# Optimization experiments

Hardware: AMD Instinct MI355X
Metric: run time of the kernel (lower is better)

Reference implementation:

```python
import jax, jax.numpy as jnp
import numpy as np
from jax import lax

V, Dm, NL, N, K, E = 32000, 1024, 4, 16, 4, 2
Di = Dm * E
B, T = 1, 2048
EPS = 1e-5


def setup_inputs() -> dict:
    key = jax.random.key(0)
    ks = jax.random.split(key, 8)
    s = 0.02
    A_init = jnp.log(jnp.arange(1.0, N + 1, dtype=jnp.float32))  # (N,)
    return {
        "idx": jax.random.randint(ks[0], (B, T), 0, V),
        "emb": jax.random.normal(ks[1], (V, Dm), dtype=jnp.float32) * s,
        "norm_w": jnp.ones((NL, Dm), jnp.float32),
        "in_proj_w": jax.random.normal(ks[2], (NL, 2 * Di, Dm), dtype=jnp.float32) * s,
        "conv_w": jax.random.normal(ks[3], (NL, Di, 1, K), dtype=jnp.float32) * s,
        "conv_b": jnp.zeros((NL, Di), jnp.float32),
        "x_proj_w": jax.random.normal(ks[4], (NL, 2 * N + 1, Di), dtype=jnp.float32) * s,
        "dt_proj_w": jax.random.normal(ks[5], (NL, Di, 1), dtype=jnp.float32) * s,
        "dt_proj_b": jnp.zeros((NL, Di), jnp.float32),
        "A_log": jnp.broadcast_to(A_init[None, None, :], (NL, Di, N)).copy(),
        "D_param": jnp.ones((NL, Di), jnp.float32),
        "out_proj_w": jax.random.normal(ks[6], (NL, Dm, Di), dtype=jnp.float32) * s,
        "norm_f_w": jnp.ones((Dm,), jnp.float32),
    }


def _rmsnorm(x, w):
    rms = jnp.sqrt(jnp.mean(x * x, axis=-1, keepdims=True) + EPS)
    return x / rms * w


def _mamba_block(x, in_w, cw, cb, xp_w, dt_w, dt_b, A_log, Dp, out_w):
    # x: (B, L, Dm)
    xz = x @ in_w.T                       # (B, L, 2*Di)
    x_ssm, z = xz[..., :Di], xz[..., Di:]
    # causal depthwise conv (torch pads both sides then crops -> left-pad only)
    xc = x_ssm.transpose(0, 2, 1)         # (B, Di, L)
    xc = lax.conv_general_dilated(
        xc, cw, window_strides=(1,), padding=[(K - 1, 0)],
        dimension_numbers=("NCH", "OIH", "NCH"), feature_group_count=Di)
    xc = xc + cb[None, :, None]
    u = jax.nn.silu(xc.transpose(0, 2, 1))  # (B, L, Di)
    # selective SSM
    A = -jnp.exp(A_log)                     # (Di, N)
    xp = u @ xp_w.T                         # (B, L, 2N+1)
    dt_raw, Bv, Cv = xp[..., :1], xp[..., 1:1 + N], xp[..., 1 + N:]
    dt = jax.nn.softplus(dt_raw * dt_w[:, 0] + dt_b)  # (B, L, Di)

    def step(h, inp):
        dt_t, Bv_t, Cv_t, u_t = inp          # (B,Di),(B,N),(B,N),(B,Di)
        dA = jnp.exp(dt_t[..., None] * A)    # (B, Di, N)
        h = dA * h + (dt_t * u_t)[..., None] * Bv_t[:, None, :]
        y_t = jnp.einsum("bdn,bn->bd", h, Cv_t)
        return h, y_t

    h0 = jnp.zeros((x.shape[0], Di, N), u.dtype)
    xs = (dt.transpose(1, 0, 2), Bv.transpose(1, 0, 2),
          Cv.transpose(1, 0, 2), u.transpose(1, 0, 2))
    _, ys = lax.scan(step, h0, xs)           # (L, B, Di)
    y = ys.transpose(1, 0, 2) + u * Dp
    y = y * jax.nn.silu(z)
    return y @ out_w.T


def reference(idx, emb, norm_w, in_proj_w, conv_w, conv_b, x_proj_w,
              dt_proj_w, dt_proj_b, A_log, D_param, out_proj_w, norm_f_w):
    x = emb[idx]                             # (B, T, Dm); dropout=0 in eval
    for l in range(NL):
        x = x + _mamba_block(_rmsnorm(x, norm_w[l]), in_proj_w[l], conv_w[l],
                             conv_b[l], x_proj_w[l], dt_proj_w[l], dt_proj_b[l],
                             A_log[l], D_param[l], out_proj_w[l])
    x = _rmsnorm(x, norm_f_w)
    logits = x @ emb.T                       # tied lm_head
    return logits
```

## Files before the change

kernel.cpp:

```cpp
#include <hip/hip_runtime.h>
#include <hip/hip_bf16.h>

typedef __hip_bfloat16 bf16;
typedef __attribute__((ext_vector_type(8))) short short8;
typedef __attribute__((ext_vector_type(4))) float f32x4;

#define TT 2048
#define DM 1024
#define DI 2048
#define NLAYER 4
#define NST 16
#define KC 4
#define VOCAB 32000
#define XPS 33
#define NCHUNK 64
#define CLEN 32

__device__ __forceinline__ float us2f(unsigned short u) {
    union { float f; unsigned int i; } c; c.i = ((unsigned int)u) << 16; return c.f;
}
__device__ __forceinline__ float ldin(const void* p, size_t i, int f32) {
    return f32 ? ((const float*)p)[i] : us2f(((const unsigned short*)p)[i]);
}
__device__ __forceinline__ unsigned short f2us(float f) {
    bf16 h = __float2bfloat16(f);
    return *(unsigned short*)&h;
}
__device__ __forceinline__ size_t hidx(int n, int c, int d) {
    return ((size_t)n * NCHUNK + c) * DI + d;
}

__global__ void detect_kernel(const unsigned int* __restrict__ w_bits, int* __restrict__ flag) {
    if (threadIdx.x == 0) *flag = (w_bits[0] == 0x3F800000u) ? 1 : 0;
}

__global__ void cvt8_dual_kernel(const float* __restrict__ sA, unsigned short* __restrict__ dA, int n8A,
                                 const float* __restrict__ sB, unsigned short* __restrict__ dB, int n8B) {
    int i = blockIdx.x * 256 + threadIdx.x;
    const float* s; unsigned short* d;
    if (i < n8A) { s = sA; d = dA; }
    else { i -= n8A; if (i >= n8B) return; s = sB; d = dB; }
    float4 a = ((const float4*)s)[2 * i];
    float4 b = ((const float4*)s)[2 * i + 1];
    unsigned int w0 = (unsigned int)f2us(a.x) | ((unsigned int)f2us(a.y) << 16);
    unsigned int w1 = (unsigned int)f2us(a.z) | ((unsigned int)f2us(a.w) << 16);
    unsigned int w2 = (unsigned int)f2us(b.x) | ((unsigned int)f2us(b.y) << 16);
    unsigned int w3 = (unsigned int)f2us(b.z) | ((unsigned int)f2us(b.w) << 16);
    ((uint4*)d)[i] = make_uint4(w0, w1, w2, w3);
}

__global__ void embed_kernel(const int* __restrict__ idx, const void* __restrict__ emb,
                             float* __restrict__ x, const int* __restrict__ fl) {
    int f32 = *fl;
    int t = blockIdx.x, q = threadIdx.x;
    size_t src = (size_t)idx[t] * DM + q * 4;
    float4 v;
    if (f32) v = *(const float4*)((const float*)emb + src);
    else {
        ushort4 h = *(const ushort4*)((const unsigned short*)emb + src);
        v = make_float4(us2f(h.x), us2f(h.y), us2f(h.z), us2f(h.w));
    }
    ((float4*)x)[(size_t)t * (DM / 4) + q] = v;
}

__global__ void rmsnorm_kernel(const float* __restrict__ x, const void* __restrict__ w,
                               size_t wofs, bf16* __restrict__ ob, const int* __restrict__ fl) {
    int f32 = *fl;
    int t = blockIdx.x, tid = threadIdx.x;
    int wv = tid >> 6, lane = tid & 63;
    float4 v = ((const float4*)(x + (size_t)t * DM))[tid];
    float s = v.x * v.x + v.y * v.y + v.z * v.z + v.w * v.w;
#pragma unroll
    for (int o = 1; o < 64; o <<= 1) s += __shfl_xor(s, o, 64);
    __shared__ float red[4];
    if (lane == 0) red[wv] = s;
    __syncthreads();
    float inv = rsqrtf((red[0] + red[1] + red[2] + red[3]) / (float)DM + 1e-5f);
    float w0, w1, w2, w3;
    if (f32) {
        float4 wq = ((const float4*)((const float*)w + wofs))[tid];
        w0 = wq.x; w1 = wq.y; w2 = wq.z; w3 = wq.w;
    } else {
        ushort4 wq = ((const ushort4*)((const unsigned short*)w + wofs))[tid];
        w0 = us2f(wq.x); w1 = us2f(wq.y); w2 = us2f(wq.z); w3 = us2f(wq.w);
    }
    uint2 o;
    o.x = (unsigned int)f2us(v.x * inv * w0) | ((unsigned int)f2us(v.y * inv * w1) << 16);
    o.y = (unsigned int)f2us(v.z * inv * w2) | ((unsigned int)f2us(v.w * inv * w3) << 16);
    ((uint2*)(ob + (size_t)t * DM))[tid] = o;
}

template<int BM>
__global__ __launch_bounds__(256, 2)
void gemm_mfma(const bf16* __restrict__ A16, const bf16* __restrict__ B16,
               const float* __restrict__ Res, float* __restrict__ Cf, bf16* __restrict__ C16,
               int MT, int NT, int Kk) {
    constexpr int BK = 64;
    constexpr int MR = BM / 32;
    constexpr int AQ = BM / 32;
    int Nn = NT << 7;
    __shared__ __align__(16) char smem[(BM + 128) * BK * 2];
    unsigned short* As = (unsigned short*)smem;
    unsigned short* Bs = As + BM * BK;
    float* Cs = (float*)smem;

    int tid = threadIdx.x;
    int w = tid >> 6, lane = tid & 63;
    int h = lane >> 4, r = lane & 15;

    int nwg = MT * NT;
    int bid = blockIdx.x;
    int swz = ((nwg & 7) == 0) ? ((bid & 7) * (nwg >> 3) + (bid >> 3)) : bid;
    int mt = swz % MT, nt = swz / MT;
    int m0 = mt * BM, n0 = nt << 7;

    const unsigned short* Ap = (const unsigned short*)A16;
    const unsigned short* Bp = (const unsigned short*)B16;

    int srow = tid >> 3;
    int skof = (((tid & 7) ^ ((tid >> 3) & 7)) << 3);
    const unsigned short* gA = Ap + (size_t)(m0 + srow) * Kk + skof;
    const unsigned short* gB = Bp + (size_t)(n0 + srow) * Kk + skof;

    f32x4 acc[MR][4];
#pragma unroll
    for (int i = 0; i < MR; i++)
#pragma unroll
        for (int j = 0; j < 4; j++) acc[i][j] = (f32x4){0.f, 0.f, 0.f, 0.f};

    int wr = w >> 1, wc = w & 1;
    int rA0 = ((wr * (BM / 2)) + r) << 6;
    int rB0 = (((wc << 6)) + r) << 6;
    int cx = r & 7;

    for (int k0 = 0; k0 < Kk; k0 += BK) {
#pragma unroll
        for (int q = 0; q < AQ; q++)
            __builtin_amdgcn_global_load_lds(
                (const __attribute__((address_space(1))) void*)(gA + k0 + (size_t)(q * 32) * Kk),
                (__attribute__((address_space(3))) void*)(As + q * 2048 + (w << 9)), 16, 0, 0);
#pragma unroll
        for (int q = 0; q < 4; q++)
            __builtin_amdgcn_global_load_lds(
                (const __attribute__((address_space(1))) void*)(gB + k0 + (size_t)(q * 32) * Kk),
                (__attribute__((address_space(3))) void*)(Bs + q * 2048 + (w << 9)), 16, 0, 0);
        __syncthreads();
#pragma unroll
        for (int kk = 0; kk < 2; kk++) {
            short8 af[MR], bfr[4];
#pragma unroll
            for (int mi = 0; mi < MR; mi++)
                af[mi] = *(const short8*)(As + rA0 + (mi << 10) + ((((kk << 2) | h) ^ cx) << 3));
#pragma unroll
            for (int ni = 0; ni < 4; ni++)
                bfr[ni] = *(const short8*)(Bs + rB0 + (ni << 10) + ((((kk << 2) | h) ^ cx) << 3));
#pragma unroll
            for (int mi = 0; mi < MR; mi++)
#pragma unroll
                for (int ni = 0; ni < 4; ni++)
                    acc[mi][ni] = __builtin_amdgcn_mfma_f32_16x16x32_bf16(
                        af[mi], bfr[ni], acc[mi][ni], 0, 0, 0);
        }
        __syncthreads();
    }
#pragma unroll
    for (int p = 0; p < BM / 32; p++) {
#pragma unroll
        for (int mi = 0; mi < MR; mi++) {
            int mloc = wr * (BM / 2) + mi * 16;
            if ((mloc >> 5) != p) continue;
            int lr0 = (mloc & 31) + (h << 2);
#pragma unroll
            for (int j = 0; j < 4; j++)
#pragma unroll
                for (int ni = 0; ni < 4; ni++)
                    Cs[(lr0 + j) * 132 + (wc << 6) + (ni << 4) + r] = acc[mi][ni][j];
        }
        __syncthreads();
#pragma unroll
        for (int q2 = 0; q2 < 4; q2++) {
            int f = q2 * 256 + tid;
            int rr = f >> 5, c4 = f & 31;
            int grow = m0 + p * 32 + rr;
            size_t go = (size_t)grow * Nn + n0 + (c4 << 2);
            float4 v = *(const float4*)&Cs[rr * 132 + (c4 << 2)];
            if (Res) {
                float4 rv = *(const float4*)(Res + go);
                v.x += rv.x; v.y += rv.y; v.z += rv.z; v.w += rv.w;
            }
            if (Cf) *(float4*)(Cf + go) = v;
            if (C16) {
                uint2 o;
                o.x = (unsigned int)f2us(v.x) | ((unsigned int)f2us(v.y) << 16);
                o.y = (unsigned int)f2us(v.z) | ((unsigned int)f2us(v.w) << 16);
                *(uint2*)((unsigned short*)C16 + go) = o;
            }
        }
        __syncthreads();
    }
}

__global__ void cxp_kernel(const float* __restrict__ xz,
                           const void* __restrict__ cw, size_t cwofs,
                           const void* __restrict__ cb, size_t cbofs,
                           const void* __restrict__ xpw, size_t xpwofs,
                           float* __restrict__ u, float* __restrict__ xp,
                           const int* __restrict__ fl) {
    int f32 = *fl;
    int t = blockIdx.x, tid = threadIdx.x;
    int wv = tid >> 6, lane = tid & 63;
    int d0 = tid * 8;
    float uv[8];
#pragma unroll
    for (int k = 0; k < 8; k++) uv[k] = ldin(cb, cbofs + d0 + k, f32);
#pragma unroll
    for (int j = 0; j < KC; j++) {
        int tt = t - (KC - 1) + j;
        if (tt < 0) continue;
        const float* row = xz + (size_t)tt * (2 * DI) + d0;
        float4 v0 = *(const float4*)row;
        float4 v1 = *(const float4*)(row + 4);
        float vv[8] = {v0.x, v0.y, v0.z, v0.w, v1.x, v1.y, v1.z, v1.w};
#pragma unroll
        for (int k = 0; k < 8; k++)
            uv[k] += ldin(cw, cwofs + (size_t)(d0 + k) * KC + j, f32) * vv[k];
    }
#pragma unroll
    for (int k = 0; k < 8; k++) { float s = uv[k]; uv[k] = s / (1.f + __expf(-s)); }
    float* ur = u + (size_t)t * DI + d0;
    *(float4*)ur       = make_float4(uv[0], uv[1], uv[2], uv[3]);
    *(float4*)(ur + 4) = make_float4(uv[4], uv[5], uv[6], uv[7]);

    float p[XPS];
    if (f32) {
        const float* wb = (const float*)xpw + xpwofs + d0;
#pragma unroll
        for (int n = 0; n < XPS; n++) {
            const float* wp = wb + (size_t)n * DI;
            float4 w0 = *(const float4*)wp, w1 = *(const float4*)(wp + 4);
            p[n] = uv[0] * w0.x + uv[1] * w0.y + uv[2] * w0.z + uv[3] * w0.w
                 + uv[4] * w1.x + uv[5] * w1.y + uv[6] * w1.z + uv[7] * w1.w;
        }
    } else {
        const unsigned short* wb = (const unsigned short*)xpw + xpwofs + d0;
#pragma unroll
        for (int n = 0; n < XPS; n++) {
            uint4 wq = *(const uint4*)(wb + (size_t)n * DI);
            p[n] = uv[0] * us2f(wq.x & 0xffff) + uv[1] * us2f(wq.x >> 16)
                 + uv[2] * us2f(wq.y & 0xffff) + uv[3] * us2f(wq.y >> 16)
                 + uv[4] * us2f(wq.z & 0xffff) + uv[5] * us2f(wq.z >> 16)
                 + uv[6] * us2f(wq.w & 0xffff) + uv[7] * us2f(wq.w >> 16);
        }
    }
    __shared__ float red[4 * XPS];
#pragma unroll
    for (int n = 0; n < XPS; n++) {
        float v = p[n];
#pragma unroll
        for (int s_ = 1; s_ < 64; s_ <<= 1) v += __shfl_xor(v, s_, 64);
        if (lane == 0) red[wv * XPS + n] = v;
    }
    __syncthreads();
    if (tid < XPS)
        xp[t * XPS + tid] = red[tid] + red[XPS + tid] + red[2 * XPS + tid] + red[3 * XPS + tid];
}

__global__ void scanA_kernel(const float* __restrict__ xp, const float* __restrict__ u,
                             const void* __restrict__ dtw, size_t dtwofs,
                             const void* __restrict__ dtb, size_t dtbofs,
                             const void* __restrict__ A_log, size_t aofs,
                             float* __restrict__ S, float* __restrict__ hend,
                             const int* __restrict__ fl) {
    int f32 = *fl;
    int c = blockIdx.y;
    int d = blockIdx.x * 256 + threadIdx.x;
    __shared__ float xps[CLEN * XPS];
    for (int i = threadIdx.x; i < CLEN * XPS; i += 256) xps[i] = xp[c * CLEN * XPS + i];
    __syncthreads();
    float dw = ldin(dtw, dtwofs + d, f32);
    float db = ldin(dtb, dtbofs + d, f32);
    float Ar[NST], hh[NST];
#pragma unroll
    for (int n = 0; n < NST; n++) {
        Ar[n] = -expf(ldin(A_log, aofs + (size_t)d * NST + n, f32));
        hh[n] = 0.f;
    }
    float ssum = 0.f;
    const float* urow = u + (size_t)c * CLEN * DI + d;
    for (int tt = 0; tt < CLEN; tt++) {
        float s = xps[tt * XPS] * dw + db;
        float dtv = (s > 20.f) ? s : log1pf(__expf(s));
        float uvv = urow[(size_t)tt * DI];
        float du = dtv * uvv;
        ssum += dtv;
        const float* bb = &xps[tt * XPS + 1];
#pragma unroll
        for (int n = 0; n < NST; n++)
            hh[n] = __expf(dtv * Ar[n]) * hh[n] + du * bb[n];
    }
    S[c * DI + d] = ssum;
#pragma unroll
    for (int n = 0; n < NST; n++) hend[hidx(n, c, d)] = hh[n];
}

__global__ void scanB_kernel(const float* __restrict__ S, float* __restrict__ hend,
                             const void* __restrict__ A_log, size_t aofs,
                             const int* __restrict__ fl) {
    int f32 = *fl;
    int i = blockIdx.x * 256 + threadIdx.x;
    int d = i & (DI - 1), n = i >> 11;
    float A = -expf(ldin(A_log, aofs + (size_t)d * NST + n, f32));
    float H = 0.f;
    for (int c = 0; c < NCHUNK; c++) {
        size_t o = hidx(n, c, d);
        float he = hend[o];
        hend[o] = H;
        H = __expf(A * S[c * DI + d]) * H + he;
    }
}

__global__ void scanC_kernel(const float* __restrict__ xp, const float* __restrict__ u,
                             const float* __restrict__ xz,
                             const void* __restrict__ dtw, size_t dtwofs,
                             const void* __restrict__ dtb, size_t dtbofs,
                             const void* __restrict__ A_log, size_t aofs,
                             const void* __restrict__ Dp, size_t dofs,
                             const float* __restrict__ hcar, bf16* __restrict__ y16,
                             const int* __restrict__ fl) {
    int f32 = *fl;
    int c = blockIdx.y;
    int d = blockIdx.x * 256 + threadIdx.x;
    __shared__ float xps[CLEN * XPS];
    for (int i = threadIdx.x; i < CLEN * XPS; i += 256) xps[i] = xp[c * CLEN * XPS + i];
    __syncthreads();
    float dw = ldin(dtw, dtwofs + d, f32);
    float db = ldin(dtb, dtbofs + d, f32);
    float Dpv = ldin(Dp, dofs + d, f32);
    float Ar[NST], hh[NST];
#pragma unroll
    for (int n = 0; n < NST; n++) {
        Ar[n] = -expf(ldin(A_log, aofs + (size_t)d * NST + n, f32));
        hh[n] = hcar[hidx(n, c, d)];
    }
    for (int tt = 0; tt < CLEN; tt++) {
        int t = c * CLEN + tt;
        float s = xps[tt * XPS] * dw + db;
        float dtv = (s > 20.f) ? s : log1pf(__expf(s));
        float uvv = u[(size_t)t * DI + d];
        float du = dtv * uvv;
        const float* bb = &xps[tt * XPS + 1];
        const float* cc = &xps[tt * XPS + 1 + NST];
        float accv = 0.f;
#pragma unroll
        for (int n = 0; n < NST; n++) {
            hh[n] = __expf(dtv * Ar[n]) * hh[n] + du * bb[n];
            accv += hh[n] * cc[n];
        }
        float z = xz[(size_t)t * (2 * DI) + DI + d];
        float sz = z / (1.f + __expf(-z));
        y16[(size_t)t * DI + d] = __float2bfloat16((accv + uvv * Dpv) * sz);
    }
}

extern "C" void kernel_launch(void* const* d_in, const int* in_sizes, int n_in,
                              void* d_out, int out_size, void* d_ws, size_t ws_size,
                              hipStream_t stream) {
    const int*  idx       = (const int*)d_in[0];
    const void* emb       = d_in[1];
    const void* norm_w    = d_in[2];
    const void* in_proj_w = d_in[3];
    const void* conv_w    = d_in[4];
    const void* conv_b    = d_in[5];
    const void* x_proj_w  = d_in[6];
    const void* dt_proj_w = d_in[7];
    const void* dt_proj_b = d_in[8];
    const void* A_log     = d_in[9];
    const void* D_param   = d_in[10];
    const void* out_proj_w= d_in[11];
    const void* norm_f_w  = d_in[12];

    float* ws   = (float*)d_ws;
    float* xz   = ws;
    float* u    = ws + 8388608;
    float* hend = ws + 12582912;
    bf16*  W16A = (bf16*)(ws + 14680064);
    bf16*  W16B = (bf16*)(ws + 16777216);
    float* S    = ws + 17825792;
    float* xp   = ws + 17956864;
    float* x    = ws + 18024448;
    bf16*  xn16 = (bf16*)(ws + 20121600);
    bf16*  y16  = (bf16*)(ws + 21170176);
    int*   fl   = (int*)(ws + 23267328);
    bf16*  emb16= (bf16*)ws;

    long long esz = in_sizes ? (long long)in_sizes[1] : -1;
    int isf32 = (esz == (long long)VOCAB * DM * 2) ? 0 : 1;

    detect_kernel<<<1, 64, 0, stream>>>((const unsigned int*)norm_w, fl);
    embed_kernel<<<TT, 256, 0, stream>>>(idx, emb, x, fl);

    for (int l = 0; l < NLAYER; l++) {
        const bf16* Bin;
        const bf16* Bout;
        if (isf32) {
            int n8A = 2 * DI * DM / 8, n8B = DM * DI / 8;
            cvt8_dual_kernel<<<(n8A + n8B + 255) / 256, 256, 0, stream>>>(
                (const float*)in_proj_w + (size_t)l * 2 * DI * DM, (unsigned short*)W16A, n8A,
                (const float*)out_proj_w + (size_t)l * DM * DI, (unsigned short*)W16B, n8B);
            Bin = W16A; Bout = W16B;
        } else {
            Bin  = (const bf16*)in_proj_w  + (size_t)l * 2 * DI * DM;
            Bout = (const bf16*)out_proj_w + (size_t)l * DM * DI;
        }

        rmsnorm_kernel<<<TT, 256, 0, stream>>>(x, norm_w, (size_t)l * DM, xn16, fl);
        gemm_mfma<64><<<(TT / 64) * (2 * DI / 128), 256, 0, stream>>>(
            xn16, Bin, nullptr, xz, nullptr, TT / 64, 2 * DI / 128, DM);
        cxp_kernel<<<TT, 256, 0, stream>>>(
            xz, conv_w, (size_t)l * DI * KC, conv_b, (size_t)l * DI,
            x_proj_w, (size_t)l * XPS * DI, u, xp, fl);
        scanA_kernel<<<dim3(DI / 256, NCHUNK), 256, 0, stream>>>(
            xp, u, dt_proj_w, (size_t)l * DI, dt_proj_b, (size_t)l * DI,
            A_log, (size_t)l * DI * NST, S, hend, fl);
        scanB_kernel<<<DI * NST / 256, 256, 0, stream>>>(
            S, hend, A_log, (size_t)l * DI * NST, fl);
        scanC_kernel<<<dim3(DI / 256, NCHUNK), 256, 0, stream>>>(
            xp, u, xz, dt_proj_w, (size_t)l * DI, dt_proj_b, (size_t)l * DI,
            A_log, (size_t)l * DI * NST, D_param, (size_t)l * DI, hend, y16, fl);
        gemm_mfma<32><<<(TT / 32) * (DM / 128), 256, 0, stream>>>(
            y16, Bout, x, x, nullptr, TT / 32, DM / 128, DI);
    }

    rmsnorm_kernel<<<TT, 256, 0, stream>>>(x, norm_f_w, 0, xn16, fl);

    const bf16* Bemb;
    if (isf32) {
        int n8 = VOCAB * DM / 8;
        cvt8_dual_kernel<<<(n8 + 255) / 256, 256, 0, stream>>>(
            (const float*)emb, (unsigned short*)emb16, n8, nullptr, nullptr, 0);
        Bemb = emb16;
    } else {
        Bemb = (const bf16*)emb;
    }
    if (isf32)
        gemm_mfma<128><<<(TT / 128) * (VOCAB / 128), 256, 0, stream>>>(
            xn16, Bemb, nullptr, (float*)d_out, nullptr, TT / 128, VOCAB / 128, DM);
    else
        gemm_mfma<128><<<(TT / 128) * (VOCAB / 128), 256, 0, stream>>>(
            xn16, Bemb, nullptr, nullptr, (bf16*)d_out, TT / 128, VOCAB / 128, DM);
}
```

Before: 1.513 ms.

## Fuse conv into scans, embed with rmsnorm, batch weight casts, retune GEMM tiles

Drops the separate u buffer and recomputes the causal conv and SiLU inside scanA and scanC from xz. Fuses the embedding lookup with the first rmsnorm and replaces the device-side dtype flag with a host-computed argument. When workspace allows, converts all layer weights and the embedding to bf16 in two up-front kernels instead of once per layer. It also raises the in_proj GEMM tile to BM=128 and the launch-bounds occupancy for small tiles. In exchange, the conv and SiLU are computed twice and more workspace is needed.

New measurement: 1.550 ms. +2.5%, slower.

```diff
diff --git a/kernel.cpp b/kernel.cpp
--- a/kernel.cpp
+++ b/kernel.cpp
@@ -28,10 +28,6 @@
 }
 __device__ __forceinline__ size_t hidx(int n, int c, int d) {
     return ((size_t)n * NCHUNK + c) * DI + d;
-}
-
-__global__ void detect_kernel(const unsigned int* __restrict__ w_bits, int* __restrict__ flag) {
-    if (threadIdx.x == 0) *flag = (w_bits[0] == 0x3F800000u) ? 1 : 0;
 }
 
 __global__ void cvt8_dual_kernel(const float* __restrict__ sA, unsigned short* __restrict__ dA, int n8A,
@@ -49,23 +45,42 @@
     ((uint4*)d)[i] = make_uint4(w0, w1, w2, w3);
 }
 
-__global__ void embed_kernel(const int* __restrict__ idx, const void* __restrict__ emb,
-                             float* __restrict__ x, const int* __restrict__ fl) {
-    int f32 = *fl;
-    int t = blockIdx.x, q = threadIdx.x;
-    size_t src = (size_t)idx[t] * DM + q * 4;
+__global__ void embed_rms_kernel(const int* __restrict__ idx, const void* __restrict__ emb,
+                                 const void* __restrict__ w, float* __restrict__ x,
+                                 bf16* __restrict__ ob, int f32) {
+    int t = blockIdx.x, tid = threadIdx.x;
+    int wv = tid >> 6, lane = tid & 63;
+    size_t src = (size_t)idx[t] * DM + tid * 4;
     float4 v;
     if (f32) v = *(const float4*)((const float*)emb + src);
     else {
         ushort4 h = *(const ushort4*)((const unsigned short*)emb + src);
         v = make_float4(us2f(h.x), us2f(h.y), us2f(h.z), us2f(h.w));
     }
-    ((float4*)x)[(size_t)t * (DM / 4) + q] = v;
+    ((float4*)x)[(size_t)t * (DM / 4) + tid] = v;
+    float s = v.x * v.x + v.y * v.y + v.z * v.z + v.w * v.w;
+#pragma unroll
+    for (int o = 1; o < 64; o <<= 1) s += __shfl_xor(s, o, 64);
+    __shared__ float red[4];
+    if (lane == 0) red[wv] = s;
+    __syncthreads();
+    float inv = rsqrtf((red[0] + red[1] + red[2] + red[3]) / (float)DM + 1e-5f);
+    float w0, w1, w2, w3;
+    if (f32) {
+        float4 wq = ((const float4*)w)[tid];
+        w0 = wq.x; w1 = wq.y; w2 = wq.z; w3 = wq.w;
+    } else {
+        ushort4 wq = ((const ushort4*)w)[tid];
+        w0 = us2f(wq.x); w1 = us2f(wq.y); w2 = us2f(wq.z); w3 = us2f(wq.w);
+    }
+    uint2 o;
+    o.x = (unsigned int)f2us(v.x * inv * w0) | ((unsigned int)f2us(v.y * inv * w1) << 16);
+    o.y = (unsigned int)f2us(v.z * inv * w2) | ((unsigned int)f2us(v.w * inv * w3) << 16);
+    ((uint2*)(ob + (size_t)t * DM))[tid] = o;
 }
 
 __global__ void rmsnorm_kernel(const float* __restrict__ x, const void* __restrict__ w,
-                               size_t wofs, bf16* __restrict__ ob, const int* __restrict__ fl) {
-    int f32 = *fl;
+                               size_t wofs, bf16* __restrict__ ob, int f32) {
     int t = blockIdx.x, tid = threadIdx.x;
     int wv = tid >> 6, lane = tid & 63;
     float4 v = ((const float4*)(x + (size_t)t * DM))[tid];
@@ -91,7 +106,7 @@
 }
 
 template<int BM>
-__global__ __launch_bounds__(256, 2)
+__global__ __launch_bounds__(256, (BM <= 64 ? 4 : 2))
 void gemm_mfma(const bf16* __restrict__ A16, const bf16* __restrict__ B16,
                const float* __restrict__ Res, float* __restrict__ Cf, bf16* __restrict__ C16,
                int MT, int NT, int Kk) {
@@ -204,9 +219,7 @@
                            const void* __restrict__ cw, size_t cwofs,
                            const void* __restrict__ cb, size_t cbofs,
                            const void* __restrict__ xpw, size_t xpwofs,
-                           float* __restrict__ u, float* __restrict__ xp,
-                           const int* __restrict__ fl) {
-    int f32 = *fl;
+                           float* __restrict__ xp, int f32) {
     int t = blockIdx.x, tid = threadIdx.x;
     int wv = tid >> 6, lane = tid & 63;
     int d0 = tid * 8;
@@ -227,9 +240,6 @@
     }
 #pragma unroll
     for (int k = 0; k < 8; k++) { float s = uv[k]; uv[k] = s / (1.f + __expf(-s)); }
-    float* ur = u + (size_t)t * DI + d0;
-    *(float4*)ur       = make_float4(uv[0], uv[1], uv[2], uv[3]);
-    *(float4*)(ur + 4) = make_float4(uv[4], uv[5], uv[6], uv[7]);
 
     float p[XPS];
     if (f32) {
@@ -265,13 +275,13 @@
         xp[t * XPS + tid] = red[tid] + red[XPS + tid] + red[2 * XPS + tid] + red[3 * XPS + tid];
 }
 
-__global__ void scanA_kernel(const float* __restrict__ xp, const float* __restrict__ u,
+__global__ void scanA_kernel(const float* __restrict__ xp, const float* __restrict__ xz,
+                             const void* __restrict__ cw, size_t cwofs,
+                             const void* __restrict__ cb, size_t cbofs,
                              const void* __restrict__ dtw, size_t dtwofs,
                              const void* __restrict__ dtb, size_t dtbofs,
                              const void* __restrict__ A_log, size_t aofs,
-                             float* __restrict__ S, float* __restrict__ hend,
-                             const int* __restrict__ fl) {
-    int f32 = *fl;
+                             float* __restrict__ S, float* __restrict__ hend, int f32) {
     int c = blockIdx.y;
     int d = blockIdx.x * 256 + threadIdx.x;
     __shared__ float xps[CLEN * XPS];
@@ -279,18 +289,29 @@
     __syncthreads();
     float dw = ldin(dtw, dtwofs + d, f32);
     float db = ldin(dtb, dtbofs + d, f32);
+    float c0 = ldin(cw, cwofs + (size_t)d * KC + 0, f32);
+    float c1 = ldin(cw, cwofs + (size_t)d * KC + 1, f32);
+    float c2 = ldin(cw, cwofs + (size_t)d * KC + 2, f32);
+    float c3 = ldin(cw, cwofs + (size_t)d * KC + 3, f32);
+    float cbv = ldin(cb, cbofs + d, f32);
     float Ar[NST], hh[NST];
 #pragma unroll
     for (int n = 0; n < NST; n++) {
         Ar[n] = -expf(ldin(A_log, aofs + (size_t)d * NST + n, f32));
         hh[n] = 0.f;
     }
+    int tb = c * CLEN;
+    float w0 = (tb >= 3) ? xz[(size_t)(tb - 3) * (2 * DI) + d] : 0.f;
+    float w1 = (tb >= 2) ? xz[(size_t)(tb - 2) * (2 * DI) + d] : 0.f;
+    float w2 = (tb >= 1) ? xz[(size_t)(tb - 1) * (2 * DI) + d] : 0.f;
     float ssum = 0.f;
-    const float* urow = u + (size_t)c * CLEN * DI + d;
     for (int tt = 0; tt < CLEN; tt++) {
+        float cur = xz[(size_t)(tb + tt) * (2 * DI) + d];
+        float s0 = cbv + c0 * w0 + c1 * w1 + c2 * w2 + c3 * cur;
+        float uvv = s0 / (1.f + __expf(-s0));
+        w0 = w1; w1 = w2; w2 = cur;
         float s = xps[tt * XPS] * dw + db;
         float dtv = (s > 20.f) ? s : log1pf(__expf(s));
-        float uvv = urow[(size_t)tt * DI];
         float du = dtv * uvv;
         ssum += dtv;
         const float* bb = &xps[tt * XPS + 1];
@@ -304,9 +325,7 @@
 }
 
 __global__ void scanB_kernel(const float* __restrict__ S, float* __restrict__ hend,
-                             const void* __restrict__ A_log, size_t aofs,
-                             const int* __restrict__ fl) {
-    int f32 = *fl;
+                             const void* __restrict__ A_log, size_t aofs, int f32) {
     int i = blockIdx.x * 256 + threadIdx.x;
     int d = i & (DI - 1), n = i >> 11;
     float A = -expf(ldin(A_log, aofs + (size_t)d * NST + n, f32));
@@ -319,15 +338,14 @@
     }
 }
 
-__global__ void scanC_kernel(const float* __restrict__ xp, const float* __restrict__ u,
-                             const float* __restrict__ xz,
+__global__ void scanC_kernel(const float* __restrict__ xp, const float* __restrict__ xz,
+                             const void* __restrict__ cw, size_t cwofs,
+                             const void* __restrict__ cb, size_t cbofs,
                              const void* __restrict__ dtw, size_t dtwofs,
                              const void* __restrict__ dtb, size_t dtbofs,
                              const void* __restrict__ A_log, size_t aofs,
                              const void* __restrict__ Dp, size_t dofs,
-                             const float* __restrict__ hcar, bf16* __restrict__ y16,
-                             const int* __restrict__ fl) {
-    int f32 = *fl;
+                             const float* __restrict__ hcar, bf16* __restrict__ y16, int f32) {
     int c = blockIdx.y;
     int d = blockIdx.x * 256 + threadIdx.x;
     __shared__ float xps[CLEN * XPS];
@@ -336,17 +354,29 @@
     float dw = ldin(dtw, dtwofs + d, f32);
     float db = ldin(dtb, dtbofs + d, f32);
     float Dpv = ldin(Dp, dofs + d, f32);
+    float c0 = ldin(cw, cwofs + (size_t)d * KC + 0, f32);
+    float c1 = ldin(cw, cwofs + (size_t)d * KC + 1, f32);
+    float c2 = ldin(cw, cwofs + (size_t)d * KC + 2, f32);
+    float c3 = ldin(cw, cwofs + (size_t)d * KC + 3, f32);
+    float cbv = ldin(cb, cbofs + d, f32);
     float Ar[NST], hh[NST];
 #pragma unroll
     for (int n = 0; n < NST; n++) {
         Ar[n] = -expf(ldin(A_log, aofs + (size_t)d * NST + n, f32));
         hh[n] = hcar[hidx(n, c, d)];
     }
+    int tb = c * CLEN;
+    float w0 = (tb >= 3) ? xz[(size_t)(tb - 3) * (2 * DI) + d] : 0.f;
+    float w1 = (tb >= 2) ? xz[(size_t)(tb - 2) * (2 * DI) + d] : 0.f;
+    float w2 = (tb >= 1) ? xz[(size_t)(tb - 1) * (2 * DI) + d] : 0.f;
     for (int tt = 0; tt < CLEN; tt++) {
-        int t = c * CLEN + tt;
+        int t = tb + tt;
+        float cur = xz[(size_t)t * (2 * DI) + d];
+        float s0 = cbv + c0 * w0 + c1 * w1 + c2 * w2 + c3 * cur;
+        float uvv = s0 / (1.f + __expf(-s0));
+        w0 = w1; w1 = w2; w2 = cur;
         float s = xps[tt * XPS] * dw + db;
         float dtv = (s > 20.f) ? s : log1pf(__expf(s));
-        float uvv = u[(size_t)t * DI + d];
         float du = dtv * uvv;
         const float* bb = &xps[tt * XPS + 1];
         const float* cc = &xps[tt * XPS + 1 + NST];
@@ -381,7 +411,6 @@
 
     float* ws   = (float*)d_ws;
     float* xz   = ws;
-    float* u    = ws + 8388608;
     float* hend = ws + 12582912;
     bf16*  W16A = (bf16*)(ws + 14680064);
     bf16*  W16B = (bf16*)(ws + 16777216);
@@ -390,57 +419,78 @@
     float* x    = ws + 18024448;
     bf16*  xn16 = (bf16*)(ws + 20121600);
     bf16*  y16  = (bf16*)(ws + 21170176);
-    int*   fl   = (int*)(ws + 23267328);
-    bf16*  emb16= (bf16*)ws;
+    bf16*  embOv= (bf16*)ws;
+    bf16*  WinAll = (bf16*)(ws + 23268352);
+    bf16*  WoutAll= (bf16*)(ws + 31656960);
+    bf16*  EmbAll = (bf16*)(ws + 35851264);
+    const size_t need_upfront = (size_t)52235264 * 4;
 
     long long esz = in_sizes ? (long long)in_sizes[1] : -1;
     int isf32 = (esz == (long long)VOCAB * DM * 2) ? 0 : 1;
-
-    detect_kernel<<<1, 64, 0, stream>>>((const unsigned int*)norm_w, fl);
-    embed_kernel<<<TT, 256, 0, stream>>>(idx, emb, x, fl);
+    int upfront = isf32 && (ws_size >= need_upfront);
+
+    if (upfront) {
+        int n8A = NLAYER * 2 * DI * DM / 8, n8B = NLAYER * DM * DI / 8;
+        cvt8_dual_kernel<<<(n8A + n8B + 255) / 256, 256, 0, stream>>>(
+            (const float*)in_proj_w, (unsigned short*)WinAll, n8A,
+            (const float*)out_proj_w, (unsigned short*)WoutAll, n8B);
+        int n8E = VOCAB * DM / 8;
+        cvt8_dual_kernel<<<(n8E + 255) / 256, 256, 0, stream>>>(
+            (const float*)emb, (unsigned short*)EmbAll, n8E, nullptr, nullptr, 0);
+    }
+
+    embed_rms_kernel<<<TT, 256, 0, stream>>>(idx, emb, norm_w, x, xn16, isf32);
 
     for (int l = 0; l < NLAYER; l++) {
         const bf16* Bin;
         const bf16* Bout;
-        if (isf32) {
+        if (!isf32) {
+            Bin  = (const bf16*)in_proj_w  + (size_t)l * 2 * DI * DM;
+            Bout = (const bf16*)out_proj_w + (size_t)l * DM * DI;
+        } else if (upfront) {
+            Bin  = WinAll  + (size_t)l * 2 * DI * DM;
+            Bout = WoutAll + (size_t)l * DM * DI;
+        } else {
             int n8A = 2 * DI * DM / 8, n8B = DM * DI / 8;
             cvt8_dual_kernel<<<(n8A + n8B + 255) / 256, 256, 0, stream>>>(
                 (const float*)in_proj_w + (size_t)l * 2 * DI * DM, (unsigned short*)W16A, n8A,
                 (const float*)out_proj_w + (size_t)l * DM * DI, (unsigned short*)W16B, n8B);
             Bin = W16A; Bout = W16B;
-        } else {
-            Bin  = (const bf16*)in_proj_w  + (size_t)l * 2 * DI * DM;
-            Bout = (const bf16*)out_proj_w + (size_t)l * DM * DI;
-        }
-
-        rmsnorm_kernel<<<TT, 256, 0, stream>>>(x, norm_w, (size_t)l * DM, xn16, fl);
-        gemm_mfma<64><<<(TT / 64) * (2 * DI / 128), 256, 0, stream>>>(
-            xn16, Bin, nullptr, xz, nullptr, TT / 64, 2 * DI / 128, DM);
+        }
+
+        if (l > 0)
+            rmsnorm_kernel<<<TT, 256, 0, stream>>>(x, norm_w, (size_t)l * DM, xn16, isf32);
+        gemm_mfma<128><<<(TT / 128) * (2 * DI / 128), 256, 0, stream>>>(
+            xn16, Bin, nullptr, xz, nullptr, TT / 128, 2 * DI / 128, DM);
         cxp_kernel<<<TT, 256, 0, stream>>>(
             xz, conv_w, (size_t)l * DI * KC, conv_b, (size_t)l * DI,
-            x_proj_w, (size_t)l * XPS * DI, u, xp, fl);
+            x_proj_w, (size_t)l * XPS * DI, xp, isf32);
         scanA_kernel<<<dim3(DI / 256, NCHUNK), 256, 0, stream>>>(
-            xp, u, dt_proj_w, (size_t)l * DI, dt_proj_b, (size_t)l * DI,
-            A_log, (size_t)l * DI * NST, S, hend, fl);
+            xp, xz, conv_w, (size_t)l * DI * KC, conv_b, (size_t)l * DI,
+            dt_proj_w, (size_t)l * DI, dt_proj_b, (size_t)l * DI,
+            A_log, (size_t)l * DI * NST, S, hend, isf32);
         scanB_kernel<<<DI * NST / 256, 256, 0, stream>>>(
-            S, hend, A_log, (size_t)l * DI * NST, fl);
+            S, hend, A_log, (size_t)l * DI * NST, isf32);
         scanC_kernel<<<dim3(DI / 256, NCHUNK), 256, 0, stream>>>(
-            xp, u, xz, dt_proj_w, (size_t)l * DI, dt_proj_b, (size_t)l * DI,
-            A_log, (size_t)l * DI * NST, D_param, (size_t)l * DI, hend, y16, fl);
+            xp, xz, conv_w, (size_t)l * DI * KC, conv_b, (size_t)l * DI,
+            dt_proj_w, (size_t)l * DI, dt_proj_b, (size_t)l * DI,
+            A_log, (size_t)l * DI * NST, D_param, (size_t)l * DI, hend, y16, isf32);
         gemm_mfma<32><<<(TT / 32) * (DM / 128), 256, 0, stream>>>(
             y16, Bout, x, x, nullptr, TT / 32, DM / 128, DI);
     }
 
-    rmsnorm_kernel<<<TT, 256, 0, stream>>>(x, norm_f_w, 0, xn16, fl);
+    rmsnorm_kernel<<<TT, 256, 0, stream>>>(x, norm_f_w, 0, xn16, isf32);
 
     const bf16* Bemb;
-    if (isf32) {
+    if (!isf32) {
+        Bemb = (const bf16*)emb;
+    } else if (upfront) {
+        Bemb = EmbAll;
+    } else {
         int n8 = VOCAB * DM / 8;
         cvt8_dual_kernel<<<(n8 + 255) / 256, 256, 0, stream>>>(
-            (const float*)emb, (unsigned short*)emb16, n8, nullptr, nullptr, 0);
-        Bemb = emb16;
-    } else {
-        Bemb = (const bf16*)emb;
+            (const float*)emb, (unsigned short*)embOv, n8, nullptr, nullptr, 0);
+        Bemb = embOv;
     }
     if (isf32)
         gemm_mfma<128><<<(TT / 128) * (VOCAB / 128), 256, 0, stream>>>(
```
